# Kernel tuning notes

Hardware: AMD Instinct MI355X
Metric: run time of the kernel (lower is better)

Reference implementation:

```python
import jax, jax.numpy as jnp
import numpy as np

B, L, H = 64, 512, 512
LOC_SIZE = 100000
EPS = 1e-9
STDV = 1.0 / np.sqrt(H)


def _uniform(key, shape):
    return jax.random.uniform(key, shape, dtype=jnp.float32, minval=-STDV, maxval=STDV)


def setup_inputs() -> dict:
    key = jax.random.key(0)
    ks = jax.random.split(key, 16)
    return {
        "td_upper": jax.random.uniform(ks[0], (B, L), dtype=jnp.float32),
        "td_lower": jax.random.uniform(ks[1], (B, L), dtype=jnp.float32),
        "ld_upper": jax.random.uniform(ks[2], (B, L), dtype=jnp.float32),
        "ld_lower": jax.random.uniform(ks[3], (B, L), dtype=jnp.float32),
        "current_loc": jax.random.randint(ks[4], (B, L), 0, LOC_SIZE, dtype=jnp.int64)
            if jax.config.jax_enable_x64 else jax.random.randint(ks[4], (B, L), 0, LOC_SIZE).astype(jnp.int32),
        "loc_len": jax.random.randint(ks[5], (B,), 0, L).astype(jnp.int32),
        "weight_ih": _uniform(ks[6], (H, H)),
        "weight_th_upper": _uniform(ks[7], (H, H)),
        "weight_th_lower": _uniform(ks[8], (H, H)),
        "weight_sh_upper": _uniform(ks[9], (H, H)),
        "weight_sh_lower": _uniform(ks[10], (H, H)),
        "h0": _uniform(ks[11], (H, 1)),
        "location_weight": _uniform(ks[12], (LOC_SIZE, H)),
    }


def reference(td_upper, td_lower, ld_upper, ld_lower, current_loc, loc_len,
              weight_ih, weight_th_upper, weight_th_lower,
              weight_sh_upper, weight_sh_lower, h0, location_weight):
    # per-step mixing coefficients [B, L]
    td_den = td_upper + td_lower + EPS
    a = td_upper / td_den
    b = td_lower / td_den
    ld_den = ld_upper + ld_lower + EPS
    c = ld_upper / ld_den
    d = ld_lower / ld_den

    loc = location_weight[current_loc]  # [B, L, H]

    # ttd_j @ loc_j = a_j * (Wtu @ loc_j) + b_j * (Wtl @ loc_j)
    vt = (a[..., None] * jnp.einsum('blh,kh->blk', loc, weight_th_upper)
          + b[..., None] * jnp.einsum('blh,kh->blk', loc, weight_th_lower))
    # sld_j @ vt_j
    term = (c[..., None] * jnp.einsum('blh,kh->blk', vt, weight_sh_upper)
            + d[..., None] * jnp.einsum('blh,kh->blk', vt, weight_sh_lower))

    mask = (jnp.arange(term.shape[1])[None, :] < loc_len[:, None])  # [B, L]
    loc_vec = jnp.sum(term * mask[..., None].astype(term.dtype), axis=1)  # [B, H]

    usr_vec = (weight_ih @ h0)[:, 0]  # [H]
    return jax.nn.softmax(loc_vec + usr_vec[None, :], axis=1)
```

## Files before the change

kernel.cpp:

```cpp
#include <hip/hip_runtime.h>
#include <math.h>

constexpr int NB = 64;
constexpr int NL = 512;
constexpr int NH = 512;
#define EPSV 1e-9f


__global__ __launch_bounds__(256) void k1_gather(
    const float* __restrict__ td_u, const float* __restrict__ td_l,
    const float* __restrict__ ld_u, const float* __restrict__ ld_l,
    const int* __restrict__ cur_loc, const int* __restrict__ loc_len,
    const float* __restrict__ locw, float* __restrict__ S)
{
    const int b   = blockIdx.y;
    const int len = loc_len[b];
    const int l0  = blockIdx.x * 32;
    if (l0 >= len) return;
    const int l1  = min(l0 + 32, len);

    const int tid = threadIdx.x;
    const int hi  = tid & 127;
    const int ls  = tid >> 7;

    float acc[4][4];
#pragma unroll
    for (int a = 0; a < 4; ++a)
#pragma unroll
        for (int e = 0; e < 4; ++e) acc[a][e] = 0.f;

#pragma unroll 4
    for (int l = l0 + ls; l < l1; l += 2) {
        const int off = b * NL + l;
        const float tu = td_u[off], tl = td_l[off];
        const float lu = ld_u[off], ll = ld_l[off];
        const float rt = 1.f / (tu + tl + EPSV);
        const float rl = 1.f / (lu + ll + EPSV);
        const float a_ = tu * rt, b_ = tl * rt;
        const float c_ = lu * rl, d_ = ll * rl;
        const float w[4] = { c_ * a_, c_ * b_, d_ * a_, d_ * b_ };
        const int idx = cur_loc[off];
        const float4 x = *(const float4*)(locw + (size_t)idx * NH + hi * 4);
#pragma unroll
        for (int a = 0; a < 4; ++a) {
            acc[a][0] += w[a] * x.x;
            acc[a][1] += w[a] * x.y;
            acc[a][2] += w[a] * x.z;
            acc[a][3] += w[a] * x.w;
        }
    }

    __shared__ float comb[128][16];
    if (ls == 1) {
#pragma unroll
        for (int a = 0; a < 4; ++a)
#pragma unroll
            for (int e = 0; e < 4; ++e) comb[hi][a * 4 + e] = acc[a][e];
    }
    __syncthreads();
    if (ls == 0) {
#pragma unroll
        for (int a = 0; a < 4; ++a)
#pragma unroll
            for (int e = 0; e < 4; ++e) {
                const float v = acc[a][e] + comb[hi][a * 4 + e];
                atomicAdd(&S[a * (NH * NB) + (hi * 4 + e) * NB + b], v);
            }
    }
}

__global__ __launch_bounds__(256) void k2_vt(
    const float* __restrict__ Wtu, const float* __restrict__ Wtl,
    const float* __restrict__ S,
    float* __restrict__ Vc, float* __restrict__ Vd)
{
    const int j   = blockIdx.x;
    const int tid = threadIdx.x;

    __shared__ float wu_s[NH];
    __shared__ float wl_s[NH];
    __shared__ float comb[4][2][NB];

    {
        const float2 va = ((const float2*)(Wtu + (size_t)j * NH))[tid];
        const float2 vb = ((const float2*)(Wtl + (size_t)j * NH))[tid];
        ((float2*)wu_s)[tid] = va;
        ((float2*)wl_s)[tid] = vb;
    }
    __syncthreads();

    const int w    = tid >> 6;
    const int lane = tid & 63;
    const float* __restrict__ Sca = S;
    const float* __restrict__ Scb = S + NH * NB;
    const float* __restrict__ Sda = S + 2 * NH * NB;
    const float* __restrict__ Sdb = S + 3 * NH * NB;

    float vc0 = 0.f, vc1 = 0.f, vd0 = 0.f, vd1 = 0.f;
    const int hbeg = w * 128;
#pragma unroll 8
    for (int h = hbeg; h < hbeg + 128; h += 2) {
        const float wuA = wu_s[h],     wlA = wl_s[h];
        const float wuB = wu_s[h + 1], wlB = wl_s[h + 1];
        const int oA = h * NB + lane;
        const int oB = oA + NB;
        vc0 += wuA * Sca[oA] + wlA * Scb[oA];
        vd0 += wuA * Sda[oA] + wlA * Sdb[oA];
        vc1 += wuB * Sca[oB] + wlB * Scb[oB];
        vd1 += wuB * Sda[oB] + wlB * Sdb[oB];
    }
    comb[w][0][lane] = vc0 + vc1;
    comb[w][1][lane] = vd0 + vd1;
    __syncthreads();

    if (tid < NB) {
        Vc[j * NB + tid] = comb[0][0][tid] + comb[1][0][tid]
                         + comb[2][0][tid] + comb[3][0][tid];
    } else if (tid < 2 * NB) {
        const int ln = tid - NB;
        Vd[j * NB + ln] = comb[0][1][ln] + comb[1][1][ln]
                        + comb[2][1][ln] + comb[3][1][ln];
    }
}

__global__ __launch_bounds__(256) void k3_logits(
    const float* __restrict__ Wsu, const float* __restrict__ Wsl,
    const float* __restrict__ Wih, const float* __restrict__ h0p,
    const float* __restrict__ Vc, const float* __restrict__ Vd,
    float* __restrict__ lg)
{
    const int j   = blockIdx.x;
    const int tid = threadIdx.x;

    __shared__ float su_s[NH];
    __shared__ float sl_s[NH];
    __shared__ float ih_s[NH];
    __shared__ float h0_s[NH];
    __shared__ float comb[4][64];
    __shared__ float comb_u[4];

    {
        const float2 va = ((const float2*)(Wsu + (size_t)j * NH))[tid];
        const float2 vb = ((const float2*)(Wsl + (size_t)j * NH))[tid];
        const float2 vi = ((const float2*)(Wih + (size_t)j * NH))[tid];
        const float2 vh = ((const float2*)h0p)[tid];
        ((float2*)su_s)[tid] = va;
        ((float2*)sl_s)[tid] = vb;
        ((float2*)ih_s)[tid] = vi;
        ((float2*)h0_s)[tid] = vh;
    }
    __syncthreads();

    const int w    = tid >> 6;
    const int lane = tid & 63;

    float s0 = 0.f, s1 = 0.f, u = 0.f;
    const int kbeg = w * 128;
#pragma unroll 8
    for (int k = kbeg; k < kbeg + 128; k += 2) {
        const float aA = su_s[k],     cA = sl_s[k];
        const float aB = su_s[k + 1], cB = sl_s[k + 1];
        const int oA = k * NB + lane;
        const int oB = oA + NB;
        s0 += aA * Vc[oA] + cA * Vd[oA];
        s1 += aB * Vc[oB] + cB * Vd[oB];
        u  += ih_s[k] * h0_s[k] + ih_s[k + 1] * h0_s[k + 1];
    }
    comb[w][lane] = s0 + s1;
    if (lane == 0) comb_u[w] = u;
    __syncthreads();

    if (tid < NB) {
        const float s = comb[0][tid] + comb[1][tid] + comb[2][tid] + comb[3][tid];
        const float usr = comb_u[0] + comb_u[1] + comb_u[2] + comb_u[3];
        lg[j * NB + tid] = s + usr;
    }
}

__global__ __launch_bounds__(512) void k4_softmax(
    const float* __restrict__ lg, float* __restrict__ out)
{
    const int b = blockIdx.x;
    const int j = threadIdx.x;
    __shared__ float sd[512];

    const float v = lg[j * NB + b];
    sd[j] = v;
    __syncthreads();
    for (int s = 256; s > 0; s >>= 1) {
        if (j < s) sd[j] = fmaxf(sd[j], sd[j + s]);
        __syncthreads();
    }
    const float m = sd[0];
    __syncthreads();
    const float e = expf(v - m);
    sd[j] = e;
    __syncthreads();
    for (int s = 256; s > 0; s >>= 1) {
        if (j < s) sd[j] += sd[j + s];
        __syncthreads();
    }
    const float denom = sd[0];
    out[b * NH + j] = e / denom;
}

extern "C" void kernel_launch(void* const* d_in, const int* in_sizes, int n_in,
                              void* d_out, int out_size, void* d_ws, size_t ws_size,
                              hipStream_t stream)
{
    const float* td_u = (const float*)d_in[0];
    const float* td_l = (const float*)d_in[1];
    const float* ld_u = (const float*)d_in[2];
    const float* ld_l = (const float*)d_in[3];
    const int*   cloc = (const int*)d_in[4];
    const int*   llen = (const int*)d_in[5];
    const float* Wih  = (const float*)d_in[6];
    const float* Wtu  = (const float*)d_in[7];
    const float* Wtl  = (const float*)d_in[8];
    const float* Wsu  = (const float*)d_in[9];
    const float* Wsl  = (const float*)d_in[10];
    const float* h0   = (const float*)d_in[11];
    const float* locw = (const float*)d_in[12];

    float* S  = (float*)d_ws;
    float* Vc = S  + 4 * NH * NB;
    float* Vd = Vc + NH * NB;
    float* lg = Vd + NH * NB;
    float* out = (float*)d_out;

    hipMemsetAsync(S, 0, (size_t)4 * NH * NB * sizeof(float), stream);

    k1_gather<<<dim3(NL / 32, NB), 256, 0, stream>>>(
        td_u, td_l, ld_u, ld_l, cloc, llen, locw, S);
    k2_vt<<<NH, 256, 0, stream>>>(Wtu, Wtl, S, Vc, Vd);
    k3_logits<<<NH, 256, 0, stream>>>(Wsu, Wsl, Wih, h0, Vc, Vd, lg);
    k4_softmax<<<NB, 512, 0, stream>>>(lg, out);
}
```

Measured before the change: 363.1 us.

## Partition gather kernel over hidden dim instead of sequence, drop atomics and memset

The gather kernel now gives each block a 32-wide slice of the hidden dimension and loops over the whole sequence, so every output element has exactly one writer. This removes the global atomicAdds and the workspace memset launch. Partial sums are reduced with wave shuffles and a small shared-memory pass. In exchange, each row index and the four coefficient arrays are re-read by 16 blocks. Each row fetch is now a 128-byte segment instead of a full 2KB row, and the coefficient divides are recomputed per block.

```diff
diff --git a/kernel.cpp b/kernel.cpp
--- a/kernel.cpp
+++ b/kernel.cpp
@@ -13,15 +13,13 @@
     const int* __restrict__ cur_loc, const int* __restrict__ loc_len,
     const float* __restrict__ locw, float* __restrict__ S)
 {
+    const int hc  = blockIdx.x;
     const int b   = blockIdx.y;
     const int len = loc_len[b];
-    const int l0  = blockIdx.x * 32;
-    if (l0 >= len) return;
-    const int l1  = min(l0 + 32, len);
-
     const int tid = threadIdx.x;
-    const int hi  = tid & 127;
-    const int ls  = tid >> 7;
+    const int hi  = tid & 7;
+    const int ls  = tid >> 3;
+    const int hbase = hc * 32 + hi * 4;
 
     float acc[4][4];
 #pragma unroll
@@ -30,7 +28,7 @@
         for (int e = 0; e < 4; ++e) acc[a][e] = 0.f;
 
 #pragma unroll 4
-    for (int l = l0 + ls; l < l1; l += 2) {
+    for (int l = ls; l < len; l += 32) {
         const int off = b * NL + l;
         const float tu = td_u[off], tl = td_l[off];
         const float lu = ld_u[off], ll = ld_l[off];
@@ -40,7 +38,7 @@
         const float c_ = lu * rl, d_ = ll * rl;
         const float w[4] = { c_ * a_, c_ * b_, d_ * a_, d_ * b_ };
         const int idx = cur_loc[off];
-        const float4 x = *(const float4*)(locw + (size_t)idx * NH + hi * 4);
+        const float4 x = *(const float4*)(locw + (size_t)idx * NH + hbase);
 #pragma unroll
         for (int a = 0; a < 4; ++a) {
             acc[a][0] += w[a] * x.x;
@@ -50,22 +48,35 @@
         }
     }
 
-    __shared__ float comb[128][16];
-    if (ls == 1) {
+#pragma unroll
+    for (int a = 0; a < 4; ++a)
+#pragma unroll
+        for (int e = 0; e < 4; ++e) {
+            float x = acc[a][e];
+            x += __shfl_down(x, 32);
+            x += __shfl_down(x, 16);
+            x += __shfl_down(x, 8);
+            acc[a][e] = x;
+        }
+
+    __shared__ float red[4][8][17];
+    const int wv   = tid >> 6;
+    const int lane = tid & 63;
+    if (lane < 8) {
 #pragma unroll
         for (int a = 0; a < 4; ++a)
 #pragma unroll
-            for (int e = 0; e < 4; ++e) comb[hi][a * 4 + e] = acc[a][e];
-    }
-    __syncthreads();
-    if (ls == 0) {
-#pragma unroll
-        for (int a = 0; a < 4; ++a)
-#pragma unroll
-            for (int e = 0; e < 4; ++e) {
-                const float v = acc[a][e] + comb[hi][a * 4 + e];
-                atomicAdd(&S[a * (NH * NB) + (hi * 4 + e) * NB + b], v);
-            }
+            for (int e = 0; e < 4; ++e) red[wv][hi][a * 4 + e] = acc[a][e];
+    }
+    __syncthreads();
+
+    if (tid < 128) {
+        const int hi2 = tid & 7;
+        const int v   = tid >> 3;
+        const float s = red[0][hi2][v] + red[1][hi2][v]
+                      + red[2][hi2][v] + red[3][hi2][v];
+        const int a = v >> 2, e = v & 3;
+        S[a * (NH * NB) + (hc * 32 + hi2 * 4 + e) * NB + b] = s;
     }
 }
 
@@ -228,9 +239,7 @@
     float* lg = Vd + NH * NB;
     float* out = (float*)d_out;
 
-    hipMemsetAsync(S, 0, (size_t)4 * NH * NB * sizeof(float), stream);
-
-    k1_gather<<<dim3(NL / 32, NB), 256, 0, stream>>>(
+    k1_gather<<<dim3(NH / 32, NB), 256, 0, stream>>>(
         td_u, td_l, ld_u, ld_l, cloc, llen, locw, S);
     k2_vt<<<NH, 256, 0, stream>>>(Wtu, Wtl, S, Vc, Vd);
     k3_logits<<<NH, 256, 0, stream>>>(Wsu, Wsl, Wih, h0, Vc, Vd, lg);
```

Measured after the change: 311.1 us. -14.3%, faster.
